# Kernel tuning notes

Hardware: AMD Instinct MI355X
Metric: run time of the kernel (lower is better)

Reference implementation:

```python
import jax, jax.numpy as jnp
import numpy as np

HIDDEN_DIM = 128
NEIGHBOR_K = 2
N_ROWS = 1_000_000
BATCH = 262_144


def setup_inputs() -> dict:
    key = jax.random.key(0)
    k1, k2, k3, k4 = jax.random.split(key, 4)
    D = HIDDEN_DIM
    cat = D * (2 * NEIGHBOR_K + 1)  # 640
    x_rows = jax.random.normal(k1, (N_ROWS, D), dtype=jnp.float32)
    seed_indices = jax.random.randint(k2, (BATCH,), 0, N_ROWS)
    # torch.nn.Linear params: W [out, in], b [out]
    W1 = jax.random.normal(k3, (D, cat), dtype=jnp.float32) * (1.0 / np.sqrt(cat))
    b1 = jnp.zeros((D,), dtype=jnp.float32)
    W2 = jax.random.normal(k4, (D, D), dtype=jnp.float32) * (1.0 / np.sqrt(D))
    b2 = jnp.zeros((D,), dtype=jnp.float32)
    return {"x_rows": x_rows, "seed_indices": seed_indices,
            "W1": W1, "b1": b1, "W2": W2, "b2": b2}


def reference(x_rows, seed_indices, W1, b1, W2, b2):
    N, D = x_rows.shape
    B = seed_indices.shape[0]
    offsets = jnp.arange(-NEIGHBOR_K, NEIGHBOR_K + 1)  # [2k+1]
    idx = jnp.clip(seed_indices[:, None] + offsets[None, :], 0, N - 1)  # [B, 2k+1]
    # gather neighbor rows and flatten -> same as torch.cat(chunks, dim=-1)
    x_cat = x_rows[idx].reshape(B, (2 * NEIGHBOR_K + 1) * D)  # [B, 5D]
    h = jax.nn.relu(x_cat @ W1.T + b1)  # [B, D]
    return h @ W2.T + b2  # [B, D]
```

## Files before the change

kernel.cpp:

```cpp
#include <hip/hip_runtime.h>
#include <hip/hip_bf16.h>

#define D 128
#define CAT 640
#define BM 32
#define W1F_ELEMS 81920
#define W2F_ELEMS 16384

typedef __attribute__((ext_vector_type(8))) short bf16x8;
typedef __attribute__((ext_vector_type(4))) short short4v;
typedef __attribute__((ext_vector_type(4))) float f32x4;

static __device__ __forceinline__ unsigned short f32_to_bf16(float f) {
    unsigned u = __float_as_uint(f);
    unsigned r = u + 0x7FFFu + ((u >> 16) & 1u);
    return (unsigned short)(r >> 16);
}

__global__ void prep_frags(const float* __restrict__ W1, const float* __restrict__ W2,
                           unsigned short* __restrict__ W1f, unsigned short* __restrict__ W2f) {
    int f = blockIdx.x * 256 + threadIdx.x;
    if (f < W1F_ELEMS) {
        int e = f & 7, l = (f >> 3) & 63, j16 = (f >> 9) & 7, ks = f >> 12;
        int o = j16 * 16 + (l & 15);
        int k = ks * 32 + ((l >> 4) << 3) + e;
        W1f[f] = f32_to_bf16(W1[o * CAT + k]);
    } else if (f < W1F_ELEMS + W2F_ELEMS) {
        int f2 = f - W1F_ELEMS;
        int e = f2 & 7, l = (f2 >> 3) & 63, j16 = (f2 >> 9) & 7, ks = f2 >> 12;
        int o = j16 * 16 + (l & 15);
        int k = ks * 32 + ((l >> 4) << 3) + e;
        W2f[f2] = f32_to_bf16(W2[o * D + k]);
    }
}

__global__ __launch_bounds__(256) void rowmlp_kernel(
    const float* __restrict__ x_rows, const int* __restrict__ seeds,
    const unsigned short* __restrict__ W1f, const float* __restrict__ b1,
    const unsigned short* __restrict__ W2f, const float* __restrict__ b2,
    float* __restrict__ out, int Nrows)
{
    __shared__ __align__(16) unsigned short Ab[2][BM][D];
    __shared__ __align__(16) unsigned short Hb[BM][D];
    __shared__ int sseed[BM];

    const int tid = threadIdx.x;
    const int blk = blockIdx.x;

    if (tid < BM) sseed[tid] = seeds[blk * BM + tid];
    __syncthreads();

    const int grow = tid >> 3;
    const int gcol = (tid & 7) * 16;
    const float* xb = x_rows;
    const bf16x8* W1v = (const bf16x8*)W1f;
    const bf16x8* W2v = (const bf16x8*)W2f;

    const int l   = tid & 63;
    const int l15 = l & 15;
    const int lhi = l >> 4;
    const int wm  = (tid >> 7) & 1;
    const int wn  = (tid >> 6) & 1;
    const int arow = wm * 16 + l15;
    const int aswz = (arow & 7) << 3;

#define STAGE(J, BUF)                                                          \
    {                                                                          \
        int idx = sseed[grow] + (J) - 2;                                       \
        idx = idx < 0 ? 0 : (idx >= Nrows ? Nrows - 1 : idx);                  \
        const float4* src = (const float4*)(xb + (size_t)idx * D + gcol);      \
        float4 v0 = src[0], v1 = src[1], v2 = src[2], v3 = src[3];             \
        unsigned short* dr = Ab[BUF][grow];                                    \
        const int s = (grow & 7) << 3;                                         \
        short4v p;                                                             \
        p[0]=(short)f32_to_bf16(v0.x); p[1]=(short)f32_to_bf16(v0.y);          \
        p[2]=(short)f32_to_bf16(v0.z); p[3]=(short)f32_to_bf16(v0.w);          \
        *(short4v*)(&dr[(gcol + 0) ^ s]) = p;                                  \
        p[0]=(short)f32_to_bf16(v1.x); p[1]=(short)f32_to_bf16(v1.y);          \
        p[2]=(short)f32_to_bf16(v1.z); p[3]=(short)f32_to_bf16(v1.w);          \
        *(short4v*)(&dr[(gcol + 4) ^ s]) = p;                                  \
        p[0]=(short)f32_to_bf16(v2.x); p[1]=(short)f32_to_bf16(v2.y);          \
        p[2]=(short)f32_to_bf16(v2.z); p[3]=(short)f32_to_bf16(v2.w);          \
        *(short4v*)(&dr[(gcol + 8) ^ s]) = p;                                  \
        p[0]=(short)f32_to_bf16(v3.x); p[1]=(short)f32_to_bf16(v3.y);          \
        p[2]=(short)f32_to_bf16(v3.z); p[3]=(short)f32_to_bf16(v3.w);          \
        *(short4v*)(&dr[(gcol + 12) ^ s]) = p;                                 \
    }

    f32x4 acc[4] = {};

    STAGE(0, 0)
    __syncthreads();

    #pragma unroll
    for (int j = 0; j < 5; ++j) {
        const int cur = j & 1;
        if (j < 4) STAGE(j + 1, cur ^ 1)
        #pragma unroll
        for (int ks = 0; ks < 4; ++ks) {
            bf16x8 a = *(const bf16x8*)(&Ab[cur][arow][(ks * 32 + lhi * 8) ^ aswz]);
            #pragma unroll
            for (int n = 0; n < 4; ++n) {
                const int j16 = wn * 4 + n;
                bf16x8 b = W1v[((j * 4 + ks) * 8 + j16) * 64 + l];
                acc[n] = __builtin_amdgcn_mfma_f32_16x16x32_bf16(a, b, acc[n], 0, 0, 0);
            }
        }
        __syncthreads();
    }

    #pragma unroll
    for (int n = 0; n < 4; ++n) {
        const int col = wn * 64 + n * 16 + l15;
        const float bias = b1[col];
        #pragma unroll
        for (int r = 0; r < 4; ++r) {
            const int row = wm * 16 + lhi * 4 + r;
            float v = acc[n][r] + bias;
            v = v > 0.f ? v : 0.f;
            Hb[row][col ^ ((row & 7) << 3)] = f32_to_bf16(v);
        }
        acc[n] = (f32x4){0.f, 0.f, 0.f, 0.f};
    }
    __syncthreads();

    #pragma unroll
    for (int ks = 0; ks < 4; ++ks) {
        bf16x8 a = *(const bf16x8*)(&Hb[arow][(ks * 32 + lhi * 8) ^ aswz]);
        #pragma unroll
        for (int n = 0; n < 4; ++n) {
            const int j16 = wn * 4 + n;
            bf16x8 b = W2v[(ks * 8 + j16) * 64 + l];
            acc[n] = __builtin_amdgcn_mfma_f32_16x16x32_bf16(a, b, acc[n], 0, 0, 0);
        }
    }

    #pragma unroll
    for (int n = 0; n < 4; ++n) {
        const int col = wn * 64 + n * 16 + l15;
        const float bias = b2[col];
        #pragma unroll
        for (int r = 0; r < 4; ++r) {
            const int row = wm * 16 + lhi * 4 + r;
            out[(size_t)(blk * BM + row) * D + col] = acc[n][r] + bias;
        }
    }
#undef STAGE
}

extern "C" void kernel_launch(void* const* d_in, const int* in_sizes, int n_in,
                              void* d_out, int out_size, void* d_ws, size_t ws_size,
                              hipStream_t stream) {
    const float* x_rows = (const float*)d_in[0];
    const int*   seeds  = (const int*)d_in[1];
    const float* W1     = (const float*)d_in[2];
    const float* b1     = (const float*)d_in[3];
    const float* W2     = (const float*)d_in[4];
    const float* b2     = (const float*)d_in[5];
    float* out = (float*)d_out;

    int Nrows = in_sizes[0] / D;
    int B = in_sizes[1];

    unsigned short* W1f = (unsigned short*)d_ws;
    unsigned short* W2f = W1f + W1F_ELEMS;

    prep_frags<<<(W1F_ELEMS + W2F_ELEMS + 255) / 256, 256, 0, stream>>>(W1, W2, W1f, W2f);
    rowmlp_kernel<<<B / BM, 256, 0, stream>>>(x_rows, seeds, W1f, b1, W2f, b2, out, Nrows);
}
```

Baseline: 224.5 us.

## Gather all five neighbor rows up front and split work over eight waves

Replaces the double-buffered per-neighbor staging loop with one bulk gather of all 5x128 neighbor columns into a 32x640 bf16 LDS tile, using coalesced 32-lane float4 row loads. The block grows to 512 threads (8 waves, 2x4 tiling), so each wave computes 32 output columns instead of 64. This removes the per-step barriers and issues all global loads at once for more memory parallelism. In exchange LDS use rises to about 48KB per block and the gather no longer overlaps MFMA work within a block, relying on other resident blocks to hide latency.

After: 213.0 us. -5.1%, faster.

```diff
diff --git a/kernel.cpp b/kernel.cpp
--- a/kernel.cpp
+++ b/kernel.cpp
@@ -34,13 +34,13 @@
     }
 }
 
-__global__ __launch_bounds__(256) void rowmlp_kernel(
+__global__ __launch_bounds__(512, 6) void rowmlp_kernel(
     const float* __restrict__ x_rows, const int* __restrict__ seeds,
     const unsigned short* __restrict__ W1f, const float* __restrict__ b1,
     const unsigned short* __restrict__ W2f, const float* __restrict__ b2,
     float* __restrict__ out, int Nrows)
 {
-    __shared__ __align__(16) unsigned short Ab[2][BM][D];
+    __shared__ __align__(16) unsigned short Ab[BM][CAT];
     __shared__ __align__(16) unsigned short Hb[BM][D];
     __shared__ int sseed[BM];
 
@@ -50,68 +50,53 @@
     if (tid < BM) sseed[tid] = seeds[blk * BM + tid];
     __syncthreads();
 
-    const int grow = tid >> 3;
-    const int gcol = (tid & 7) * 16;
-    const float* xb = x_rows;
+    {
+        const int lane32 = tid & 31;
+        const int segbase = tid >> 5;
+        #pragma unroll
+        for (int it = 0; it < 10; ++it) {
+            int seg = it * 16 + segbase;
+            int row = seg / 5;
+            int j = seg - row * 5;
+            int idx = sseed[row] + j - 2;
+            idx = idx < 0 ? 0 : (idx >= Nrows ? Nrows - 1 : idx);
+            float4 v = *((const float4*)(x_rows + (size_t)idx * D) + lane32);
+            short4v p;
+            p[0] = (short)f32_to_bf16(v.x); p[1] = (short)f32_to_bf16(v.y);
+            p[2] = (short)f32_to_bf16(v.z); p[3] = (short)f32_to_bf16(v.w);
+            int kshort = j * D + lane32 * 4;
+            *(short4v*)(&Ab[row][kshort ^ ((row & 7) << 3)]) = p;
+        }
+    }
+    __syncthreads();
+
+    const int wave = tid >> 6;
+    const int wm   = wave >> 2;
+    const int wn   = wave & 3;
+    const int l    = tid & 63;
+    const int l15  = l & 15;
+    const int lhi  = l >> 4;
+    const int arow = wm * 16 + l15;
+    const int aswz = (arow & 7) << 3;
+
     const bf16x8* W1v = (const bf16x8*)W1f;
     const bf16x8* W2v = (const bf16x8*)W2f;
 
-    const int l   = tid & 63;
-    const int l15 = l & 15;
-    const int lhi = l >> 4;
-    const int wm  = (tid >> 7) & 1;
-    const int wn  = (tid >> 6) & 1;
-    const int arow = wm * 16 + l15;
-    const int aswz = (arow & 7) << 3;
-
-#define STAGE(J, BUF)                                                          \
-    {                                                                          \
-        int idx = sseed[grow] + (J) - 2;                                       \
-        idx = idx < 0 ? 0 : (idx >= Nrows ? Nrows - 1 : idx);                  \
-        const float4* src = (const float4*)(xb + (size_t)idx * D + gcol);      \
-        float4 v0 = src[0], v1 = src[1], v2 = src[2], v3 = src[3];             \
-        unsigned short* dr = Ab[BUF][grow];                                    \
-        const int s = (grow & 7) << 3;                                         \
-        short4v p;                                                             \
-        p[0]=(short)f32_to_bf16(v0.x); p[1]=(short)f32_to_bf16(v0.y);          \
-        p[2]=(short)f32_to_bf16(v0.z); p[3]=(short)f32_to_bf16(v0.w);          \
-        *(short4v*)(&dr[(gcol + 0) ^ s]) = p;                                  \
-        p[0]=(short)f32_to_bf16(v1.x); p[1]=(short)f32_to_bf16(v1.y);          \
-        p[2]=(short)f32_to_bf16(v1.z); p[3]=(short)f32_to_bf16(v1.w);          \
-        *(short4v*)(&dr[(gcol + 4) ^ s]) = p;                                  \
-        p[0]=(short)f32_to_bf16(v2.x); p[1]=(short)f32_to_bf16(v2.y);          \
-        p[2]=(short)f32_to_bf16(v2.z); p[3]=(short)f32_to_bf16(v2.w);          \
-        *(short4v*)(&dr[(gcol + 8) ^ s]) = p;                                  \
-        p[0]=(short)f32_to_bf16(v3.x); p[1]=(short)f32_to_bf16(v3.y);          \
-        p[2]=(short)f32_to_bf16(v3.z); p[3]=(short)f32_to_bf16(v3.w);          \
-        *(short4v*)(&dr[(gcol + 12) ^ s]) = p;                                 \
-    }
-
-    f32x4 acc[4] = {};
-
-    STAGE(0, 0)
-    __syncthreads();
-
+    f32x4 acc[2] = {};
     #pragma unroll
-    for (int j = 0; j < 5; ++j) {
-        const int cur = j & 1;
-        if (j < 4) STAGE(j + 1, cur ^ 1)
+    for (int ks = 0; ks < 20; ++ks) {
+        bf16x8 a = *(const bf16x8*)(&Ab[arow][(ks * 32 + lhi * 8) ^ aswz]);
         #pragma unroll
-        for (int ks = 0; ks < 4; ++ks) {
-            bf16x8 a = *(const bf16x8*)(&Ab[cur][arow][(ks * 32 + lhi * 8) ^ aswz]);
-            #pragma unroll
-            for (int n = 0; n < 4; ++n) {
-                const int j16 = wn * 4 + n;
-                bf16x8 b = W1v[((j * 4 + ks) * 8 + j16) * 64 + l];
-                acc[n] = __builtin_amdgcn_mfma_f32_16x16x32_bf16(a, b, acc[n], 0, 0, 0);
-            }
+        for (int n = 0; n < 2; ++n) {
+            const int j16 = wn * 2 + n;
+            bf16x8 b = W1v[(ks * 8 + j16) * 64 + l];
+            acc[n] = __builtin_amdgcn_mfma_f32_16x16x32_bf16(a, b, acc[n], 0, 0, 0);
         }
-        __syncthreads();
     }
 
     #pragma unroll
-    for (int n = 0; n < 4; ++n) {
-        const int col = wn * 64 + n * 16 + l15;
+    for (int n = 0; n < 2; ++n) {
+        const int col = wn * 32 + n * 16 + l15;
         const float bias = b1[col];
         #pragma unroll
         for (int r = 0; r < 4; ++r) {
@@ -128,16 +113,16 @@
     for (int ks = 0; ks < 4; ++ks) {
         bf16x8 a = *(const bf16x8*)(&Hb[arow][(ks * 32 + lhi * 8) ^ aswz]);
         #pragma unroll
-        for (int n = 0; n < 4; ++n) {
-            const int j16 = wn * 4 + n;
+        for (int n = 0; n < 2; ++n) {
+            const int j16 = wn * 2 + n;
             bf16x8 b = W2v[(ks * 8 + j16) * 64 + l];
             acc[n] = __builtin_amdgcn_mfma_f32_16x16x32_bf16(a, b, acc[n], 0, 0, 0);
         }
     }
 
     #pragma unroll
-    for (int n = 0; n < 4; ++n) {
-        const int col = wn * 64 + n * 16 + l15;
+    for (int n = 0; n < 2; ++n) {
+        const int col = wn * 32 + n * 16 + l15;
         const float bias = b2[col];
         #pragma unroll
         for (int r = 0; r < 4; ++r) {
@@ -145,7 +130,6 @@
             out[(size_t)(blk * BM + row) * D + col] = acc[n][r] + bias;
         }
     }
-#undef STAGE
 }
 
 extern "C" void kernel_launch(void* const* d_in, const int* in_sizes, int n_in,
@@ -166,5 +150,5 @@
     unsigned short* W2f = W1f + W1F_ELEMS;
 
     prep_frags<<<(W1F_ELEMS + W2F_ELEMS + 255) / 256, 256, 0, stream>>>(W1, W2, W1f, W2f);
-    rowmlp_kernel<<<B / BM, 256, 0, stream>>>(x_rows, seeds, W1f, b1, W2f, b2, out, Nrows);
+    rowmlp_kernel<<<B / BM, 512, 0, stream>>>(x_rows, seeds, W1f, b1, W2f, b2, out, Nrows);
 }
```
